# Kernel tuning notes

Measured on AMD Instinct MI355X. Metric: run time of the kernel, lower is better.

Reference implementation:

```python
import jax, jax.numpy as jnp
import numpy as np

NUM_HEADS = 32
ROPE_BASE = 10000.0
MASK_NEG = -66504.0  # from (1 - tril) * -66504.0 in the source


def _rotate_half(x):
    d = x.shape[-1] // 2
    return jnp.concatenate([-x[..., d:], x[..., :d]], axis=-1)


def setup_inputs() -> dict:
    key = jax.random.key(0)
    k1, k2, k3, k4 = jax.random.split(key, 4)
    S, B, E = 2048, 2, 2048
    return {
        "hidden_states": jax.random.normal(k1, (S, B, E), dtype=jnp.float32) * 0.02,
        "qkv_w": jax.random.normal(k2, (E, 3 * E), dtype=jnp.float32) * 0.02,
        "qkv_b": jax.random.normal(k3, (3 * E,), dtype=jnp.float32) * 0.02,
        "out_w": jax.random.normal(k4, (E, E), dtype=jnp.float32) * 0.02,
        "out_b": jnp.zeros((E,), dtype=jnp.float32),
    }


def reference(hidden_states, qkv_w, qkv_b, out_w, out_b):
    # seq-first prompt/prefill path of IPEXTransformerAtten
    S, B, E = hidden_states.shape
    H = NUM_HEADS
    D = E // H

    # fused QKV projection (mm_qkv_out)
    qkv = jnp.einsum('sbe,ef->sbf', hidden_states, qkv_w) + qkv_b  # [S,B,3E]
    q, k, v = jnp.split(qkv, 3, axis=-1)
    q = q.reshape(S, B, H, D)
    k = k.reshape(S, B, H, D)
    v = v.reshape(S, B, H, D)

    # rotary embedding (GPT-NeoX style, full head_dim)
    inv_freq = 1.0 / (ROPE_BASE ** (jnp.arange(0, D, 2, dtype=jnp.float32) / D))
    freqs = jnp.arange(S, dtype=jnp.float32)[:, None] * inv_freq  # [S, D/2]
    emb = jnp.concatenate([freqs, freqs], axis=-1)  # [S, D]
    cos = jnp.cos(emb)[:, None, None, :].astype(hidden_states.dtype)
    sin = jnp.sin(emb)[:, None, None, :].astype(hidden_states.dtype)
    q = q * cos + _rotate_half(q) * sin
    k = k * cos + _rotate_half(k) * sin

    # scaled dot-product attention with causal mask
    scale = 1.0 / jnp.sqrt(jnp.array(D, dtype=hidden_states.dtype))
    scores = jnp.einsum('sbhd,tbhd->bhst', q, k) * scale  # [B,H,S,S]
    causal = jnp.tril(jnp.ones((S, S), dtype=scores.dtype))
    scores = scores + (1.0 - causal) * MASK_NEG
    attn = jax.nn.softmax(scores, axis=-1)
    ctx = jnp.einsum('bhst,tbhd->sbhd', attn, v).reshape(S, B, E)

    # output projection
    return jnp.einsum('sbe,ef->sbf', ctx, out_w) + out_b
```

## Files before the change

kernel.cpp:

```cpp
#include <hip/hip_runtime.h>
#include <hip/hip_bf16.h>

#define S_LEN 2048
#define BATCH 2
#define EMB   2048
#define NH    32
#define HD    64
#define M_ROWS (S_LEN * BATCH)
#define QKV_N  (3 * EMB)

typedef short bf16x8 __attribute__((ext_vector_type(8)));
typedef float f32x4  __attribute__((ext_vector_type(4)));

__device__ __forceinline__ unsigned short f2bf(float f) {
  unsigned int u = __float_as_uint(f);
  u += 0x7fffu + ((u >> 16) & 1u);
  return (unsigned short)(u >> 16);
}
__device__ __forceinline__ float bf2f(unsigned short h) {
  return __uint_as_float(((unsigned int)h) << 16);
}
__device__ __forceinline__ void async_copy16(const void* g, void* lds) {
  __builtin_amdgcn_global_load_lds(
      (const __attribute__((address_space(1))) void*)g,
      (__attribute__((address_space(3))) void*)lds, 16, 0, 0);
}

#if __has_builtin(__builtin_amdgcn_exp2f)
#define EXP2F(x) __builtin_amdgcn_exp2f(x)
#else
#define EXP2F(x) __expf((x) * 0.6931471805599453f)
#endif


__global__ __launch_bounds__(256) void cast_to_bf16(
    const float* __restrict__ in, unsigned short* __restrict__ out, int n4) {
  int i = blockIdx.x * 256 + threadIdx.x;
  if (i >= n4) return;
  float4 v = reinterpret_cast<const float4*>(in)[i];
  ushort4 o;
  o.x = f2bf(v.x); o.y = f2bf(v.y); o.z = f2bf(v.z); o.w = f2bf(v.w);
  reinterpret_cast<ushort4*>(out)[i] = o;
}

__global__ __launch_bounds__(256) void transpose_cast2(
    const float* __restrict__ qkv_w, const float* __restrict__ out_w,
    unsigned short* __restrict__ qkvwT, unsigned short* __restrict__ outwT) {
  __shared__ float tile[32][33];
  const int z = blockIdx.z;
  const int C = z ? EMB : QKV_N;
  const int bc = blockIdx.x * 32;
  if (bc >= C) return;
  const float* in = z ? out_w : qkv_w;
  unsigned short* out = z ? outwT : qkvwT;
  const int br = blockIdx.y * 32;
  const int tx = threadIdx.x & 31, ty = threadIdx.x >> 5;
  #pragma unroll
  for (int rr = ty; rr < 32; rr += 8)
    tile[rr][tx] = in[(size_t)(br + rr) * C + bc + tx];
  __syncthreads();
  #pragma unroll
  for (int rr = ty; rr < 32; rr += 8)
    out[(size_t)(bc + rr) * EMB + br + tx] = f2bf(tile[tx][rr]);
}


__global__ __launch_bounds__(256) void gemm_qkv(
    const unsigned short* __restrict__ A,
    const unsigned short* __restrict__ Wt,
    const float* __restrict__ bias,
    unsigned short* __restrict__ Qo,
    unsigned short* __restrict__ Ko,
    unsigned short* __restrict__ Vo) {
  __shared__ __align__(16) unsigned short As[128 * 64];
  __shared__ __align__(16) unsigned short Bs[128 * 64];
  const int tid = threadIdx.x;
  const int n0 = blockIdx.x * 128;
  const int m0 = blockIdx.y * 128;
  const int wave = tid >> 6, lane = tid & 63;
  const int wm = (wave >> 1) * 64, wn = (wave & 1) * 64;
  const int lm = lane & 15, lq = lane >> 4;
  const int K = 2048;

  const int srow = tid >> 3;
  const int gch  = (tid & 7) ^ (srow & 7);
  const unsigned short* Ab = A  + (size_t)(m0 + srow) * K + gch * 8;
  const unsigned short* Bb = Wt + (size_t)(n0 + srow) * K + gch * 8;

  f32x4 acc[4][4] = {};

  for (int k0 = 0; k0 < K; k0 += 64) {
    #pragma unroll
    for (int rep = 0; rep < 4; rep++) {
      async_copy16(Ab + (size_t)rep * 32 * K + k0, As + (size_t)(tid + 256 * rep) * 8);
      async_copy16(Bb + (size_t)rep * 32 * K + k0, Bs + (size_t)(tid + 256 * rep) * 8);
    }
    __syncthreads();
    #pragma unroll
    for (int ks = 0; ks < 2; ks++) {
      bf16x8 a[4], b[4];
      #pragma unroll
      for (int i = 0; i < 4; i++) {
        const int R = wm + i*16 + lm;
        a[i] = *reinterpret_cast<const bf16x8*>(
            As + (size_t)R * 64 + (((ks*4 + lq) ^ (R & 7)) * 8));
      }
      #pragma unroll
      for (int j = 0; j < 4; j++) {
        const int R = wn + j*16 + lm;
        b[j] = *reinterpret_cast<const bf16x8*>(
            Bs + (size_t)R * 64 + (((ks*4 + lq) ^ (R & 7)) * 8));
      }
      #pragma unroll
      for (int i = 0; i < 4; i++)
        #pragma unroll
        for (int j = 0; j < 4; j++)
          acc[i][j] = __builtin_amdgcn_mfma_f32_16x16x32_bf16(a[i], b[j], acc[i][j], 0, 0, 0);
    }
    __syncthreads();
  }

  const int which = n0 >> 11;
  unsigned short* dst = (which == 0) ? Qo : (which == 1) ? Ko : Vo;
  float bv[4];
  #pragma unroll
  for (int j = 0; j < 4; j++) bv[j] = bias[n0 + wn + j*16 + lm];

  if (which < 2) {
    #pragma unroll
    for (int j = 0; j < 2; j++) {
      const int n = n0 + wn + j*16 + lm;
      const int e = n & (EMB - 1), h = e >> 6, d = e & 63;
      const float invf = EXP2F((float)d * -0.4152410118609203f);
      #pragma unroll
      for (int i = 0; i < 4; i++) {
        #pragma unroll
        for (int r = 0; r < 4; r++) {
          const int m = m0 + wm + i*16 + lq*4 + r;
          const int s = m >> 1, b = m & 1;
          const float v1 = acc[i][j][r]   + bv[j];
          const float v2 = acc[i][j+2][r] + bv[j+2];
          float sn, cs;
          __sincosf((float)s * invf, &sn, &cs);
          const size_t base = (((size_t)b * NH + h) * S_LEN + s) * HD + d;
          dst[base]      = f2bf(v1 * cs - v2 * sn);
          dst[base + 32] = f2bf(v2 * cs + v1 * sn);
        }
      }
    }
  } else {
    #pragma unroll
    for (int j = 0; j < 4; j++) {
      const int n = n0 + wn + j*16 + lm;
      const int e = n & (EMB - 1), h = e >> 6, d = e & 63;
      #pragma unroll
      for (int i = 0; i < 4; i++) {
        #pragma unroll
        for (int r = 0; r < 4; r++) {
          const int m = m0 + wm + i*16 + lq*4 + r;
          const int s = m >> 1, b = m & 1;
          dst[(((size_t)b * NH + h) * S_LEN + s) * HD + d] = f2bf(acc[i][j][r] + bv[j]);
        }
      }
    }
  }
}


__global__ __launch_bounds__(256) void transpose_v(
    const unsigned short* __restrict__ V, unsigned short* __restrict__ VT) {
  __shared__ unsigned short t[64][65];
  const int bh = blockIdx.y;
  const int s0 = blockIdx.x * 64;
  const int tx = threadIdx.x & 63, ty = threadIdx.x >> 6;
  const unsigned short* src = V + ((size_t)bh * S_LEN + s0) * HD;
  #pragma unroll
  for (int r = ty; r < 64; r += 4)
    t[r][tx] = src[(size_t)r * HD + tx];
  __syncthreads();
  unsigned short* dst = VT + (size_t)bh * HD * S_LEN + s0;
  #pragma unroll
  for (int r = ty; r < 64; r += 4)
    dst[(size_t)r * S_LEN + tx] = t[tx][r];
}


__global__ __launch_bounds__(256) void attn_kernel(
    const unsigned short* __restrict__ Q,
    const unsigned short* __restrict__ K,
    const unsigned short* __restrict__ VT,
    unsigned short* __restrict__ ctx) {
  const int bh = blockIdx.x;
  const int p  = blockIdx.y;
  const int tid = threadIdx.x;
  const int wave = tid >> 6, lane = tid & 63;
  const int lm = lane & 15, lq = lane >> 4;
  const int b = bh >> 5, h = bh & 31;
  const char* Qb8 = (const char*)(Q  + (size_t)bh * S_LEN * HD);
  const char* Kb8 = (const char*)(K  + (size_t)bh * S_LEN * HD);
  const char* Vb8 = (const char*)(VT + (size_t)bh * HD * S_LEN);

  __shared__ __align__(16) unsigned short Ks[2][2][64][32];
  __shared__ __align__(16) unsigned short Vs[2][2][64][32];
  __shared__ __align__(16) unsigned short Pbuf[4][16][72];
  unsigned short* Pw = &Pbuf[wave][0][0];

  const float C = 0.18033688011112042f;
  const int rA = p * 64 + wave * 16;
  const int rB = (31 - p) * 64 + wave * 16;
  const int nt = 32 - p;

  const int srw = tid >> 2, sc16 = (tid & 3) * 16;

  bf16x8 qf[2][2];
  #pragma unroll
  for (int s = 0; s < 2; s++) {
    const int rr = (s == 0) ? rA : rB;
    #pragma unroll
    for (int ks = 0; ks < 2; ks++)
      qf[s][ks] = *reinterpret_cast<const bf16x8*>(
          Qb8 + (size_t)(rr + lm) * 128 + ks*64 + lq*16);
  }

  f32x4 O[2][4] = {};
  float l[2][4] = {};

  {
    char* kd = (char*)&Ks[0][0][0][0];
    char* vd = (char*)&Vs[0][0][0][0];
    async_copy16(Kb8 + (size_t)srw * 128      + sc16, kd        + tid*16);
    async_copy16(Kb8 + (size_t)srw * 128 + 64 + sc16, kd + 4096 + tid*16);
    async_copy16(Vb8 + (size_t)srw * 4096      + sc16, vd        + tid*16);
    async_copy16(Vb8 + (size_t)srw * 4096 + 64 + sc16, vd + 4096 + tid*16);
  }
  __syncthreads();

  for (int t = 0; t < nt; t++) {
    const int t0 = t * 64;
    const int buf = t & 1;

    if (t + 1 < nt) {
      const int t1 = t0 + 64;
      char* kd = (char*)&Ks[buf ^ 1][0][0][0];
      char* vd = (char*)&Vs[buf ^ 1][0][0][0];
      async_copy16(Kb8 + (size_t)(t1 + srw) * 128      + sc16, kd        + tid*16);
      async_copy16(Kb8 + (size_t)(t1 + srw) * 128 + 64 + sc16, kd + 4096 + tid*16);
      async_copy16(Vb8 + (size_t)srw * 4096 + t1*2      + sc16, vd        + tid*16);
      async_copy16(Vb8 + (size_t)srw * 4096 + t1*2 + 64 + sc16, vd + 4096 + tid*16);
    }

    const char* KsB = (const char*)&Ks[buf][0][0][0];
    const char* VsB = (const char*)&Vs[buf][0][0][0];

    #pragma unroll
    for (int s = 0; s < 2; s++) {
      const int rr = (s == 0) ? rA : rB;
      if (t0 <= rr + 15) {
        const bool clean = (t0 + 63 <= rr);
        const int jmax = clean ? 4 : min(4, ((rr + 15 - t0) >> 4) + 1);
        const int kslim = (jmax + 1) >> 1;

        f32x4 sc[4] = {};
        #pragma unroll
        for (int ks = 0; ks < 2; ks++) {
          bf16x8 kf[4];
          #pragma unroll
          for (int j = 0; j < 4; j++)
            if (j < jmax)
              kf[j] = *reinterpret_cast<const bf16x8*>(
                  KsB + ks*4096 + (j*16 + lm)*64 + lq*16);
          #pragma unroll
          for (int j = 0; j < 4; j++)
            if (j < jmax)
              sc[j] = __builtin_amdgcn_mfma_f32_16x16x32_bf16(
                  qf[s][ks], kf[j], sc[j], 0, 0, 0);
        }

        if (clean) {
          #pragma unroll
          for (int j = 0; j < 4; j++)
            #pragma unroll
            for (int r = 0; r < 4; r++) {
              const float pe = EXP2F(sc[j][r] * C);
              l[s][r] += pe;
              Pw[(lq*4 + r) * 72 + j*16 + lm] = f2bf(pe);
            }
        } else {
          #pragma unroll
          for (int j = 0; j < 4; j++)
            if (j < jmax)
              #pragma unroll
              for (int r = 0; r < 4; r++) {
                const int srow = rr + lq*4 + r;
                const int tcol = t0 + j*16 + lm;
                const float pe = (tcol <= srow) ? EXP2F(sc[j][r] * C) : 0.0f;
                l[s][r] += pe;
                Pw[(lq*4 + r) * 72 + j*16 + lm] = f2bf(pe);
              }
          if (jmax & 1) {
            #pragma unroll
            for (int r = 0; r < 4; r++)
              Pw[(lq*4 + r) * 72 + jmax*16 + lm] = 0;
          }
        }

        #pragma unroll
        for (int ks = 0; ks < 2; ks++) {
          if (ks < kslim) {
            bf16x8 pf = *reinterpret_cast<const bf16x8*>(Pw + lm*72 + ks*32 + lq*8);
            bf16x8 vf[4];
            #pragma unroll
            for (int j = 0; j < 4; j++)
              vf[j] = *reinterpret_cast<const bf16x8*>(
                  VsB + ks*4096 + (j*16 + lm)*64 + lq*16);
            #pragma unroll
            for (int j = 0; j < 4; j++)
              O[s][j] = __builtin_amdgcn_mfma_f32_16x16x32_bf16(
                  pf, vf[j], O[s][j], 0, 0, 0);
          }
        }
      }
    }
    __syncthreads();
  }

  #pragma unroll
  for (int s = 0; s < 2; s++) {
    const int rr = (s == 0) ? rA : rB;
    #pragma unroll
    for (int r = 0; r < 4; r++) {
      float sum = l[s][r];
      sum += __shfl_xor(sum, 1, 64);
      sum += __shfl_xor(sum, 2, 64);
      sum += __shfl_xor(sum, 4, 64);
      sum += __shfl_xor(sum, 8, 64);
      const float inv = 1.0f / sum;
      const int srow = rr + lq*4 + r;
      #pragma unroll
      for (int j = 0; j < 4; j++) {
        const int d = j*16 + lm;
        ctx[((size_t)srow * BATCH + b) * EMB + h*HD + d] = f2bf(O[s][j][r] * inv);
      }
    }
  }
}


__global__ __launch_bounds__(256) void gemm_out(
    const unsigned short* __restrict__ A,
    const unsigned short* __restrict__ Wt,
    const float* __restrict__ bias,
    float* __restrict__ out) {
  __shared__ __align__(16) unsigned short As[2][128 * 64];
  __shared__ __align__(16) unsigned short Bs[2][128 * 64];
  const int tid = threadIdx.x;
  const int n0 = blockIdx.x * 128;
  const int m0 = blockIdx.y * 128;
  const int wave = tid >> 6, lane = tid & 63;
  const int wm = (wave >> 1) * 64, wn = (wave & 1) * 64;
  const int lm = lane & 15, lq = lane >> 4;
  const int K = 2048;

  const int srow = tid >> 3;
  const int gch  = (tid & 7) ^ (srow & 7);
  const unsigned short* Ab = A  + (size_t)(m0 + srow) * K + gch * 8;
  const unsigned short* Bb = Wt + (size_t)(n0 + srow) * K + gch * 8;

  f32x4 acc[4][4] = {};

  #pragma unroll
  for (int rep = 0; rep < 4; rep++) {
    async_copy16(Ab + (size_t)rep * 32 * K, As[0] + (size_t)(tid + 256 * rep) * 8);
    async_copy16(Bb + (size_t)rep * 32 * K, Bs[0] + (size_t)(tid + 256 * rep) * 8);
  }
  __syncthreads();

  for (int kt = 0; kt < 32; kt++) {
    const int buf = kt & 1;
    if (kt + 1 < 32) {
      const int k1 = (kt + 1) * 64;
      #pragma unroll
      for (int rep = 0; rep < 4; rep++) {
        async_copy16(Ab + (size_t)rep * 32 * K + k1, As[buf ^ 1] + (size_t)(tid + 256 * rep) * 8);
        async_copy16(Bb + (size_t)rep * 32 * K + k1, Bs[buf ^ 1] + (size_t)(tid + 256 * rep) * 8);
      }
    }
    #pragma unroll
    for (int ks = 0; ks < 2; ks++) {
      bf16x8 a[4], b[4];
      #pragma unroll
      for (int i = 0; i < 4; i++) {
        const int R = wm + i*16 + lm;
        a[i] = *reinterpret_cast<const bf16x8*>(
            As[buf] + (size_t)R * 64 + (((ks*4 + lq) ^ (R & 7)) * 8));
      }
      #pragma unroll
      for (int j = 0; j < 4; j++) {
        const int R = wn + j*16 + lm;
        b[j] = *reinterpret_cast<const bf16x8*>(
            Bs[buf] + (size_t)R * 64 + (((ks*4 + lq) ^ (R & 7)) * 8));
      }
      #pragma unroll
      for (int i = 0; i < 4; i++)
        #pragma unroll
        for (int j = 0; j < 4; j++)
          acc[i][j] = __builtin_amdgcn_mfma_f32_16x16x32_bf16(a[i], b[j], acc[i][j], 0, 0, 0);
    }
    __syncthreads();
  }

  #pragma unroll
  for (int j = 0; j < 4; j++) {
    const int n = n0 + wn + j*16 + lm;
    const float bv = bias[n];
    #pragma unroll
    for (int i = 0; i < 4; i++) {
      #pragma unroll
      for (int r = 0; r < 4; r++) {
        const int m = m0 + wm + i*16 + lq*4 + r;
        out[(size_t)m * EMB + n] = acc[i][j][r] + bv;
      }
    }
  }
}


extern "C" void kernel_launch(void* const* d_in, const int* in_sizes, int n_in,
                              void* d_out, int out_size, void* d_ws, size_t ws_size,
                              hipStream_t stream) {
  const float* hidden = (const float*)d_in[0];
  const float* qkv_w  = (const float*)d_in[1];
  const float* qkv_b  = (const float*)d_in[2];
  const float* out_w  = (const float*)d_in[3];
  const float* out_b  = (const float*)d_in[4];
  float* out = (float*)d_out;

  unsigned short* ws = (unsigned short*)d_ws;
  unsigned short* hbf   = ws;
  unsigned short* qkvwT = hbf   + (size_t)M_ROWS * EMB;
  unsigned short* outwT = qkvwT + (size_t)QKV_N * EMB;
  unsigned short* Qb    = outwT + (size_t)EMB * EMB;
  unsigned short* Kb    = Qb    + (size_t)64 * S_LEN * HD;
  unsigned short* Vb    = Kb    + (size_t)64 * S_LEN * HD;
  unsigned short* VTb   = Vb    + (size_t)64 * S_LEN * HD;
  unsigned short* ctx   = VTb   + (size_t)64 * S_LEN * HD;

  cast_to_bf16<<<(M_ROWS * EMB / 4) / 256, 256, 0, stream>>>(hidden, hbf, M_ROWS * EMB / 4);
  transpose_cast2<<<dim3(QKV_N / 32, EMB / 32, 2), 256, 0, stream>>>(qkv_w, out_w, qkvwT, outwT);

  gemm_qkv<<<dim3(QKV_N / 128, M_ROWS / 128), 256, 0, stream>>>(hbf, qkvwT, qkv_b, Qb, Kb, Vb);

  transpose_v<<<dim3(S_LEN / 64, 64), 256, 0, stream>>>(Vb, VTb);

  attn_kernel<<<dim3(64, 16), 256, 0, stream>>>(Qb, Kb, VTb, ctx);

  gemm_out<<<dim3(EMB / 128, M_ROWS / 128), 256, 0, stream>>>(ctx, outwT, out_b, out);
}
```

Baseline: 420.0 us.

## Keep attention P in registers via transposed MFMA and double rows per wave

The attention kernel now computes S^T by swapping the MFMA operands, so each lane holds P values that can be packed straight into the B operand of the PV MFMA. This removes the per-wave LDS round trip for P. Each wave now handles 32 query rows per segment instead of 16, which halves the grid and reuses each K/V LDS tile for twice as many rows. The softmax scale is folded into Q in the QKV GEMM epilogue, and ctx stores are vectorised as packed bf16 pairs. The trade-offs are more register pressure and fewer blocks to fill the CUs.

```diff
diff --git a/kernel.cpp b/kernel.cpp
--- a/kernel.cpp
+++ b/kernel.cpp
@@ -17,8 +17,9 @@
   u += 0x7fffu + ((u >> 16) & 1u);
   return (unsigned short)(u >> 16);
 }
-__device__ __forceinline__ float bf2f(unsigned short h) {
-  return __uint_as_float(((unsigned int)h) << 16);
+__device__ __forceinline__ unsigned int pkbf(float a, float b) {
+  __hip_bfloat162 t = __float22bfloat162_rn(float2{a, b});
+  return *reinterpret_cast<unsigned int*>(&t);
 }
 __device__ __forceinline__ void async_copy16(const void* g, void* lds) {
   __builtin_amdgcn_global_load_lds(
@@ -127,6 +128,7 @@
   for (int j = 0; j < 4; j++) bv[j] = bias[n0 + wn + j*16 + lm];
 
   if (which < 2) {
+    const float osc = (which == 0) ? 0.18033688011112042f : 1.0f;
     #pragma unroll
     for (int j = 0; j < 2; j++) {
       const int n = n0 + wn + j*16 + lm;
@@ -143,8 +145,8 @@
           float sn, cs;
           __sincosf((float)s * invf, &sn, &cs);
           const size_t base = (((size_t)b * NH + h) * S_LEN + s) * HD + d;
-          dst[base]      = f2bf(v1 * cs - v2 * sn);
-          dst[base + 32] = f2bf(v2 * cs + v1 * sn);
+          dst[base]      = f2bf((v1 * cs - v2 * sn) * osc);
+          dst[base + 32] = f2bf((v2 * cs + v1 * sn) * osc);
         }
       }
     }
@@ -202,28 +204,27 @@
 
   __shared__ __align__(16) unsigned short Ks[2][2][64][32];
   __shared__ __align__(16) unsigned short Vs[2][2][64][32];
-  __shared__ __align__(16) unsigned short Pbuf[4][16][72];
-  unsigned short* Pw = &Pbuf[wave][0][0];
-
-  const float C = 0.18033688011112042f;
-  const int rA = p * 64 + wave * 16;
-  const int rB = (31 - p) * 64 + wave * 16;
-  const int nt = 32 - p;
+
+  const int rA = p * 128 + wave * 32;
+  const int rB = (15 - p) * 128 + wave * 32;
+  const int nt = ((15 - p) * 128 >> 6) + 2;
 
   const int srw = tid >> 2, sc16 = (tid & 3) * 16;
 
-  bf16x8 qf[2][2];
+  bf16x8 qf[2][2][2];
   #pragma unroll
   for (int s = 0; s < 2; s++) {
-    const int rr = (s == 0) ? rA : rB;
-    #pragma unroll
-    for (int ks = 0; ks < 2; ks++)
-      qf[s][ks] = *reinterpret_cast<const bf16x8*>(
-          Qb8 + (size_t)(rr + lm) * 128 + ks*64 + lq*16);
-  }
-
-  f32x4 O[2][4] = {};
-  float l[2][4] = {};
+    const int rr = s ? rB : rA;
+    #pragma unroll
+    for (int i = 0; i < 2; i++)
+      #pragma unroll
+      for (int ks = 0; ks < 2; ks++)
+        qf[s][i][ks] = *reinterpret_cast<const bf16x8*>(
+            Qb8 + (size_t)(rr + i*16 + lm) * 128 + ks*64 + lq*16);
+  }
+
+  f32x4 O[2][2][4] = {};
+  float l[2][2] = {};
 
   {
     char* kd = (char*)&Ks[0][0][0][0];
@@ -254,69 +255,84 @@
 
     #pragma unroll
     for (int s = 0; s < 2; s++) {
-      const int rr = (s == 0) ? rA : rB;
-      if (t0 <= rr + 15) {
+      const int rr = s ? rB : rA;
+      if (t0 <= rr + 31) {
         const bool clean = (t0 + 63 <= rr);
-        const int jmax = clean ? 4 : min(4, ((rr + 15 - t0) >> 4) + 1);
-        const int kslim = (jmax + 1) >> 1;
-
-        f32x4 sc[4] = {};
+        int jm[2];
+        jm[1] = clean ? 4 : (((rr + 31 - t0) >> 4) + 1);
+        jm[0] = clean ? 4 : ((t0 > rr + 15) ? 0 : (((rr + 15 - t0) >> 4) + 1));
+
+        f32x4 sc[2][4] = {};
         #pragma unroll
         for (int ks = 0; ks < 2; ks++) {
           bf16x8 kf[4];
           #pragma unroll
           for (int j = 0; j < 4; j++)
-            if (j < jmax)
+            if (j < jm[1])
               kf[j] = *reinterpret_cast<const bf16x8*>(
                   KsB + ks*4096 + (j*16 + lm)*64 + lq*16);
           #pragma unroll
-          for (int j = 0; j < 4; j++)
-            if (j < jmax)
-              sc[j] = __builtin_amdgcn_mfma_f32_16x16x32_bf16(
-                  qf[s][ks], kf[j], sc[j], 0, 0, 0);
+          for (int i = 0; i < 2; i++)
+            #pragma unroll
+            for (int j = 0; j < 4; j++)
+              if (j < jm[i])
+                sc[i][j] = __builtin_amdgcn_mfma_f32_16x16x32_bf16(
+                    kf[j], qf[s][i][ks], sc[i][j], 0, 0, 0);
         }
 
-        if (clean) {
+        unsigned int pb[2][2][4];
+        #pragma unroll
+        for (int i = 0; i < 2; i++) {
           #pragma unroll
-          for (int j = 0; j < 4; j++)
-            #pragma unroll
-            for (int r = 0; r < 4; r++) {
-              const float pe = EXP2F(sc[j][r] * C);
-              l[s][r] += pe;
-              Pw[(lq*4 + r) * 72 + j*16 + lm] = f2bf(pe);
-            }
-        } else {
-          #pragma unroll
-          for (int j = 0; j < 4; j++)
-            if (j < jmax)
+          for (int j = 0; j < 4; j++) {
+            const int w = j >> 1, rbase = (j & 1) * 2;
+            if (j < jm[i]) {
+              const bool full = clean || (t0 + j*16 + 15 <= rr + i*16);
+              float pe[4];
               #pragma unroll
               for (int r = 0; r < 4; r++) {
-                const int srow = rr + lq*4 + r;
-                const int tcol = t0 + j*16 + lm;
-                const float pe = (tcol <= srow) ? EXP2F(sc[j][r] * C) : 0.0f;
-                l[s][r] += pe;
-                Pw[(lq*4 + r) * 72 + j*16 + lm] = f2bf(pe);
+                float v = EXP2F(sc[i][j][r]);
+                if (!full) {
+                  const int tt = t0 + j*16 + lq*4 + r;
+                  const int mm = rr + i*16 + lm;
+                  v = (tt <= mm) ? v : 0.0f;
+                }
+                pe[r] = v;
               }
-          if (jmax & 1) {
-            #pragma unroll
-            for (int r = 0; r < 4; r++)
-              Pw[(lq*4 + r) * 72 + jmax*16 + lm] = 0;
+              l[s][i] += (pe[0] + pe[1]) + (pe[2] + pe[3]);
+              pb[i][w][rbase]     = pkbf(pe[0], pe[1]);
+              pb[i][w][rbase + 1] = pkbf(pe[2], pe[3]);
+            } else {
+              pb[i][w][rbase] = 0; pb[i][w][rbase + 1] = 0;
+            }
           }
         }
 
         #pragma unroll
-        for (int ks = 0; ks < 2; ks++) {
-          if (ks < kslim) {
-            bf16x8 pf = *reinterpret_cast<const bf16x8*>(Pw + lm*72 + ks*32 + lq*8);
-            bf16x8 vf[4];
+        for (int w = 0; w < 2; w++) {
+          if (t0 + w*32 <= rr + 31) {
+            bf16x8 av[4];
             #pragma unroll
-            for (int j = 0; j < 4; j++)
-              vf[j] = *reinterpret_cast<const bf16x8*>(
-                  VsB + ks*4096 + (j*16 + lm)*64 + lq*16);
+            for (int jj = 0; jj < 4; jj++) {
+              const char* vrow = VsB + w*4096 + (jj*16 + lm)*64;
+              unsigned long long q0 = *reinterpret_cast<const unsigned long long*>(vrow + lq*8);
+              unsigned long long q1 = *reinterpret_cast<const unsigned long long*>(vrow + 32 + lq*8);
+              union { unsigned long long q[2]; bf16x8 v; } u;
+              u.q[0] = q0; u.q[1] = q1;
+              av[jj] = u.v;
+            }
             #pragma unroll
-            for (int j = 0; j < 4; j++)
-              O[s][j] = __builtin_amdgcn_mfma_f32_16x16x32_bf16(
-                  pf, vf[j], O[s][j], 0, 0, 0);
+            for (int i = 0; i < 2; i++) {
+              if (jm[i] > w*2) {
+                union { unsigned int u[4]; bf16x8 v; } pu;
+                pu.u[0] = pb[i][w][0]; pu.u[1] = pb[i][w][1];
+                pu.u[2] = pb[i][w][2]; pu.u[3] = pb[i][w][3];
+                #pragma unroll
+                for (int jj = 0; jj < 4; jj++)
+                  O[s][i][jj] = __builtin_amdgcn_mfma_f32_16x16x32_bf16(
+                      av[jj], pu.v, O[s][i][jj], 0, 0, 0);
+              }
+            }
           }
         }
       }
@@ -326,20 +342,21 @@
 
   #pragma unroll
   for (int s = 0; s < 2; s++) {
-    const int rr = (s == 0) ? rA : rB;
-    #pragma unroll
-    for (int r = 0; r < 4; r++) {
-      float sum = l[s][r];
-      sum += __shfl_xor(sum, 1, 64);
-      sum += __shfl_xor(sum, 2, 64);
-      sum += __shfl_xor(sum, 4, 64);
-      sum += __shfl_xor(sum, 8, 64);
+    const int rr = s ? rB : rA;
+    #pragma unroll
+    for (int i = 0; i < 2; i++) {
+      float sum = l[s][i];
+      sum += __shfl_xor(sum, 16, 64);
+      sum += __shfl_xor(sum, 32, 64);
       const float inv = 1.0f / sum;
-      const int srow = rr + lq*4 + r;
-      #pragma unroll
-      for (int j = 0; j < 4; j++) {
-        const int d = j*16 + lm;
-        ctx[((size_t)srow * BATCH + b) * EMB + h*HD + d] = f2bf(O[s][j][r] * inv);
+      const int srow = rr + i*16 + lm;
+      #pragma unroll
+      for (int jj = 0; jj < 4; jj++) {
+        uint2 e;
+        e.x = pkbf(O[s][i][jj][0] * inv, O[s][i][jj][1] * inv);
+        e.y = pkbf(O[s][i][jj][2] * inv, O[s][i][jj][3] * inv);
+        *reinterpret_cast<uint2*>(
+            ctx + ((size_t)srow * BATCH + b) * EMB + h*HD + jj*16 + lq*4) = e;
       }
     }
   }
@@ -452,7 +469,7 @@
 
   transpose_v<<<dim3(S_LEN / 64, 64), 256, 0, stream>>>(Vb, VTb);
 
-  attn_kernel<<<dim3(64, 16), 256, 0, stream>>>(Qb, Kb, VTb, ctx);
+  attn_kernel<<<dim3(64, 8), 256, 0, stream>>>(Qb, Kb, VTb, ctx);
 
   gemm_out<<<dim3(EMB / 128, M_ROWS / 128), 256, 0, stream>>>(ctx, outwT, out_b, out);
 }
```

Result: no change. 414.2 us (-1.4%).
